# Optimization experiments

Hardware: AMD Instinct MI355X
Metric: run time of the kernel (lower is better)

The kernel has to match this reference:

```python
import jax, jax.numpy as jnp
import numpy as np

# Dims (see init_kwargs / input_specs)
B = 16            # decode batch (slots)
QH = 32           # query heads
KVH = 8           # kv heads (GQA group = QH // KVH = 4)
D = 128           # head dim
NUM_PAGES = 4096  # total pages in cache pool
TPP = 16          # tokens per page
MAX_PPS = 256     # max pages per slot -> max context 4096


def setup_inputs() -> dict:
    key = jax.random.key(0)
    k1, k2, k3, k4, k5 = jax.random.split(key, 5)
    query = jax.random.normal(k1, (B, 1, QH, D), dtype=jnp.float32)
    key_pages = jax.random.normal(k2, (KVH, NUM_PAGES, TPP, D), dtype=jnp.float32)
    value_pages = jax.random.normal(k3, (KVH, NUM_PAGES, TPP, D), dtype=jnp.float32)
    # lengths in [1, MAX_PPS*TPP) so every slot has at least one valid token
    sequence_lengths = jax.random.randint(k4, (B,), 1, MAX_PPS * TPP, dtype=jnp.int32)
    page_map = jax.random.randint(k5, (B, MAX_PPS), 0, NUM_PAGES, dtype=jnp.int32)
    return {
        "query": query,
        "key_pages": key_pages,
        "value_pages": value_pages,
        "sequence_lengths": sequence_lengths,
        "page_map": page_map,
    }


def reference(query, key_pages, value_pages, sequence_lengths, page_map):
    """Paged attention, autoregressive decode mode (q_len == 1).

    Matches pallas paged_attention semantics: gather KV pages via page_map,
    attend over the first sequence_lengths[b] tokens (no internal 1/sqrt(d)
    scaling, matching the kernel which expects a pre-scaled query).
    """
    q = jnp.squeeze(query, axis=1)
    G = QH // KVH
    q = q.reshape(B, KVH, G, D)               # GQA grouping: [B, KVH, G, D]

    # Page-table gather: [KVH, B, MAX_PPS, TPP, D] -> [B, KVH, T, D], T = MAX_PPS*TPP
    T = MAX_PPS * TPP
    k = jnp.moveaxis(key_pages[:, page_map], 1, 0).reshape(B, KVH, T, D)
    v = jnp.moveaxis(value_pages[:, page_map], 1, 0).reshape(B, KVH, T, D)

    scores = jnp.einsum("bkgd,bktd->bkgt", q, k)       # [B, KVH, G, T]
    valid = jnp.arange(T, dtype=jnp.int32)[None, :] < sequence_lengths[:, None]  # [B, T]
    neg = jnp.asarray(jnp.finfo(scores.dtype).min, scores.dtype)
    scores = jnp.where(valid[:, None, None, :], scores, neg)
    weights = jax.nn.softmax(scores, axis=-1)
    out = jnp.einsum("bkgt,bktd->bkgd", weights, v)    # [B, KVH, G, D]
    return out.reshape(B, QH, D)
```

## Files before the change

### kernel.cpp

```cpp
#include <hip/hip_runtime.h>

constexpr int B = 16;
constexpr int QH = 32;
constexpr int KVH = 8;
constexpr int G = 4;
constexpr int D = 128;
constexpr int NUM_PAGES = 4096;
constexpr int TPP = 16;
constexpr int MAX_PPS = 256;
constexpr int CHUNK = 256;
constexpr int NCHUNK = (MAX_PPS * TPP) / CHUNK;
constexpr int PPC = CHUNK / TPP;
constexpr int WSSTRIDE = D + 2;

#define NEGF (-3.0e38f)

#define RED32(p)                 \
  do {                           \
    p += __shfl_xor(p, 16);      \
    p += __shfl_xor(p, 8);       \
    p += __shfl_xor(p, 4);       \
    p += __shfl_xor(p, 2);       \
    p += __shfl_xor(p, 1);       \
  } while (0)

__global__ __launch_bounds__(256, 4)
void pa_partial(const float* __restrict__ qg, const float* __restrict__ kp,
                const float* __restrict__ vp, const int* __restrict__ lens,
                const int* __restrict__ pmap, float* __restrict__ ws) {
  const int c = blockIdx.x;
  const int kvh = blockIdx.y;
  const int b = blockIdx.z;
  const int start = c * CHUNK;
  int ntok = lens[b] - start;
  if (ntok <= 0) return;
  if (ntok > CHUNK) ntok = CHUNK;

  __shared__ int pages[PPC];
  __shared__ float sc[CHUNK * G];
  __shared__ float wred[4][4];
  __shared__ float sred[4][4];
  __shared__ float ared[4][G * D];

  const int tid = threadIdx.x;
  const int wave = tid >> 6;
  const int lane = tid & 63;
  const int half = lane >> 5;
  const int l32 = lane & 31;

  if (tid < PPC) pages[tid] = pmap[b * MAX_PPS + (start >> 4) + tid];
#pragma unroll
  for (int i = tid; i < CHUNK * G; i += 256) sc[i] = NEGF;
  __syncthreads();

  const float4 q0 = *(const float4*)(qg + (size_t)(b * QH + kvh * G + 0) * D + 4 * l32);
  const float4 q1 = *(const float4*)(qg + (size_t)(b * QH + kvh * G + 1) * D + 4 * l32);
  const float4 q2 = *(const float4*)(qg + (size_t)(b * QH + kvh * G + 2) * D + 4 * l32);
  const float4 q3 = *(const float4*)(qg + (size_t)(b * QH + kvh * G + 3) * D + 4 * l32);

  const size_t hoff = (size_t)kvh * NUM_PAGES * TPP * D;
  const float* kbase = kp + hoff;
  const float* vbase = vp + hoff;

  float m0 = NEGF, m1 = NEGF, m2 = NEGF, m3 = NEGF;

  const int iters = (ntok + 7) >> 3;
  const int tbase = wave * 2 + half;

  float4 kv = make_float4(0.f, 0.f, 0.f, 0.f);
  if (tbase < ntok) {
    const int pg = pages[tbase >> 4];
    kv = *(const float4*)(kbase + ((size_t)pg * TPP + (tbase & 15)) * D + 4 * l32);
  }
  for (int j = 0; j < iters; ++j) {
    const int t = j * 8 + tbase;
    const bool valid = (t < ntok);
    const float4 cur = kv;
    const int tn = t + 8;
    if (tn < ntok) {
      const int pg = pages[tn >> 4];
      kv = *(const float4*)(kbase + ((size_t)pg * TPP + (tn & 15)) * D + 4 * l32);
    }
    float p0 = cur.x * q0.x + cur.y * q0.y + cur.z * q0.z + cur.w * q0.w;
    float p1 = cur.x * q1.x + cur.y * q1.y + cur.z * q1.z + cur.w * q1.w;
    float p2 = cur.x * q2.x + cur.y * q2.y + cur.z * q2.z + cur.w * q2.w;
    float p3 = cur.x * q3.x + cur.y * q3.y + cur.z * q3.z + cur.w * q3.w;
    RED32(p0);
    RED32(p1);
    RED32(p2);
    RED32(p3);
    if (valid) {
      m0 = fmaxf(m0, p0);
      m1 = fmaxf(m1, p1);
      m2 = fmaxf(m2, p2);
      m3 = fmaxf(m3, p3);
      if (l32 == 0) *(float4*)(sc + t * G) = make_float4(p0, p1, p2, p3);
    }
  }
  m0 = fmaxf(m0, __shfl_xor(m0, 32));
  m1 = fmaxf(m1, __shfl_xor(m1, 32));
  m2 = fmaxf(m2, __shfl_xor(m2, 32));
  m3 = fmaxf(m3, __shfl_xor(m3, 32));
  if (lane == 0) {
    wred[wave][0] = m0;
    wred[wave][1] = m1;
    wred[wave][2] = m2;
    wred[wave][3] = m3;
  }
  __syncthreads();

  const float M0 = fmaxf(fmaxf(wred[0][0], wred[1][0]), fmaxf(wred[2][0], wred[3][0]));
  const float M1 = fmaxf(fmaxf(wred[0][1], wred[1][1]), fmaxf(wred[2][1], wred[3][1]));
  const float M2 = fmaxf(fmaxf(wred[0][2], wred[1][2]), fmaxf(wred[2][2], wred[3][2]));
  const float M3 = fmaxf(fmaxf(wred[0][3], wred[1][3]), fmaxf(wred[2][3], wred[3][3]));
  const float Ma = (tid & 1) ? M1 : M0;
  const float Mb = (tid & 1) ? M3 : M2;
  const float Mg = (tid & 2) ? Mb : Ma;

  float lsum = 0.f;
#pragma unroll
  for (int i = tid; i < CHUNK * G; i += 256) {
    const float e = __expf(sc[i] - Mg);
    sc[i] = e;
    lsum += e;
  }
  lsum += __shfl_xor(lsum, 4);
  lsum += __shfl_xor(lsum, 8);
  lsum += __shfl_xor(lsum, 16);
  lsum += __shfl_xor(lsum, 32);
  if (lane < 4) sred[wave][lane] = lsum;
  __syncthreads();

  float4 a0 = make_float4(0.f, 0.f, 0.f, 0.f);
  float4 a1 = a0, a2 = a0, a3 = a0;
  float4 vv = make_float4(0.f, 0.f, 0.f, 0.f);
  if (tbase < ntok) {
    const int pg = pages[tbase >> 4];
    vv = *(const float4*)(vbase + ((size_t)pg * TPP + (tbase & 15)) * D + 4 * l32);
  }
  for (int j = 0; j < iters; ++j) {
    const int t = j * 8 + tbase;
    const bool valid = (t < ntok);
    const float4 cur = vv;
    const int tn = t + 8;
    if (tn < ntok) {
      const int pg = pages[tn >> 4];
      vv = *(const float4*)(vbase + ((size_t)pg * TPP + (tn & 15)) * D + 4 * l32);
    }
    if (valid) {
      const float4 wv = *(const float4*)(sc + t * G);
      a0.x += wv.x * cur.x; a0.y += wv.x * cur.y; a0.z += wv.x * cur.z; a0.w += wv.x * cur.w;
      a1.x += wv.y * cur.x; a1.y += wv.y * cur.y; a1.z += wv.y * cur.z; a1.w += wv.y * cur.w;
      a2.x += wv.z * cur.x; a2.y += wv.z * cur.y; a2.z += wv.z * cur.z; a2.w += wv.z * cur.w;
      a3.x += wv.w * cur.x; a3.y += wv.w * cur.y; a3.z += wv.w * cur.z; a3.w += wv.w * cur.w;
    }
  }
  a0.x += __shfl_xor(a0.x, 32); a0.y += __shfl_xor(a0.y, 32);
  a0.z += __shfl_xor(a0.z, 32); a0.w += __shfl_xor(a0.w, 32);
  a1.x += __shfl_xor(a1.x, 32); a1.y += __shfl_xor(a1.y, 32);
  a1.z += __shfl_xor(a1.z, 32); a1.w += __shfl_xor(a1.w, 32);
  a2.x += __shfl_xor(a2.x, 32); a2.y += __shfl_xor(a2.y, 32);
  a2.z += __shfl_xor(a2.z, 32); a2.w += __shfl_xor(a2.w, 32);
  a3.x += __shfl_xor(a3.x, 32); a3.y += __shfl_xor(a3.y, 32);
  a3.z += __shfl_xor(a3.z, 32); a3.w += __shfl_xor(a3.w, 32);
  if (half == 0) {
    *(float4*)(ared[wave] + 0 * D + 4 * l32) = a0;
    *(float4*)(ared[wave] + 1 * D + 4 * l32) = a1;
    *(float4*)(ared[wave] + 2 * D + 4 * l32) = a2;
    *(float4*)(ared[wave] + 3 * D + 4 * l32) = a3;
  }
  __syncthreads();

  const size_t wsbase = ((size_t)((b * KVH + kvh) * NCHUNK + c) * G) * WSSTRIDE;
#pragma unroll
  for (int r = 0; r < 2; ++r) {
    const int idx = tid + r * 256;
    const int g = idx >> 7;
    const int d = idx & 127;
    const float v =
        ared[0][g * D + d] + ared[1][g * D + d] + ared[2][g * D + d] + ared[3][g * D + d];
    ws[wsbase + (size_t)g * WSSTRIDE + 2 + d] = v;
  }
  if (tid < 4) {
    ws[wsbase + (size_t)tid * WSSTRIDE + 0] = Mg;
    ws[wsbase + (size_t)tid * WSSTRIDE + 1] =
        sred[0][tid] + sred[1][tid] + sred[2][tid] + sred[3][tid];
  }
}

__global__ __launch_bounds__(128)
void pa_reduce(const float* __restrict__ ws, const int* __restrict__ lens,
               float* __restrict__ out) {
  const int g = blockIdx.x;
  const int kvh = blockIdx.y;
  const int b = blockIdx.z;
  const int d = threadIdx.x;
  const int nc = (lens[b] + CHUNK - 1) / CHUNK;
  float M = NEGF, L = 0.f, acc = 0.f;
  for (int c = 0; c < nc; ++c) {
    const float* p =
        ws + ((size_t)((b * KVH + kvh) * NCHUNK + c) * G + g) * WSSTRIDE;
    const float mc = p[0];
    const float lc = p[1];
    const float ac = p[2 + d];
    const float Mn = fmaxf(M, mc);
    const float so = __expf(M - Mn);
    const float se = __expf(mc - Mn);
    L = L * so + lc * se;
    acc = acc * so + ac * se;
    M = Mn;
  }
  out[(size_t)(b * QH + kvh * G + g) * D + d] = acc / L;
}

extern "C" void kernel_launch(void* const* d_in, const int* in_sizes, int n_in,
                              void* d_out, int out_size, void* d_ws, size_t ws_size,
                              hipStream_t stream) {
  (void)in_sizes; (void)n_in; (void)out_size; (void)ws_size;
  const float* q = (const float*)d_in[0];
  const float* kp = (const float*)d_in[1];
  const float* vp = (const float*)d_in[2];
  const int* lens = (const int*)d_in[3];
  const int* pmap = (const int*)d_in[4];
  float* out = (float*)d_out;
  float* ws = (float*)d_ws;

  dim3 g1(NCHUNK, KVH, B);
  pa_partial<<<g1, 256, 0, stream>>>(q, kp, vp, lens, pmap, ws);
  dim3 g2(G, KVH, B);
  pa_reduce<<<g2, 128, 0, stream>>>(ws, lens, out);
}
```

Before: 475.1 us.

## Fuse K and V passes into single-pass online softmax with lazy rescale and grid swizzle

Replaces the two-pass scheme (score all keys into shared memory, then exponentiate and accumulate V) with a single pass that loads K and V together and keeps per-wave online-softmax state. The running max is rescaled only when a new score exceeds it by more than a threshold, which avoids most rescale exponentials. Prefetch now runs two tokens ahead for both K and V. The grid is flattened and swizzled so that batch slots rotate across chunks, spreading work from unequal sequence lengths more evenly over the machine. The cost is higher register pressure and clamped page reads past the valid range, since loads are now unconditional.

```diff
diff --git a/kernel.cpp b/kernel.cpp
--- a/kernel.cpp
+++ b/kernel.cpp
@@ -14,6 +14,7 @@
 constexpr int WSSTRIDE = D + 2;
 
 #define NEGF (-3.0e38f)
+#define DEFER_T 8.0f
 
 #define RED32(p)                 \
   do {                           \
@@ -28,16 +29,19 @@
 void pa_partial(const float* __restrict__ qg, const float* __restrict__ kp,
                 const float* __restrict__ vp, const int* __restrict__ lens,
                 const int* __restrict__ pmap, float* __restrict__ ws) {
-  const int c = blockIdx.x;
-  const int kvh = blockIdx.y;
-  const int b = blockIdx.z;
+  const int f = blockIdx.x;
+  const int hi = f >> 7;
+  const int lo = f & 127;
+  const int b = ((lo & 15) + hi) & 15;
+  const int kvh = lo >> 4;
+  const int c = hi;
+
   const int start = c * CHUNK;
   int ntok = lens[b] - start;
   if (ntok <= 0) return;
   if (ntok > CHUNK) ntok = CHUNK;
 
   __shared__ int pages[PPC];
-  __shared__ float sc[CHUNK * G];
   __shared__ float wred[4][4];
   __shared__ float sred[4][4];
   __shared__ float ared[4][G * D];
@@ -49,8 +53,6 @@
   const int l32 = lane & 31;
 
   if (tid < PPC) pages[tid] = pmap[b * MAX_PPS + (start >> 4) + tid];
-#pragma unroll
-  for (int i = tid; i < CHUNK * G; i += 256) sc[i] = NEGF;
   __syncthreads();
 
   const float4 q0 = *(const float4*)(qg + (size_t)(b * QH + kvh * G + 0) * D + 4 * l32);
@@ -62,112 +64,112 @@
   const float* kbase = kp + hoff;
   const float* vbase = vp + hoff;
 
-  float m0 = NEGF, m1 = NEGF, m2 = NEGF, m3 = NEGF;
-
   const int iters = (ntok + 7) >> 3;
   const int tbase = wave * 2 + half;
 
-  float4 kv = make_float4(0.f, 0.f, 0.f, 0.f);
-  if (tbase < ntok) {
-    const int pg = pages[tbase >> 4];
-    kv = *(const float4*)(kbase + ((size_t)pg * TPP + (tbase & 15)) * D + 4 * l32);
-  }
+  auto kvoff = [&](int t) -> size_t {
+    const int pi = min(t >> 4, PPC - 1);
+    return ((size_t)pages[pi] * TPP + (t & 15)) * D + 4 * l32;
+  };
+
+  float m0 = NEGF, m1 = NEGF, m2 = NEGF, m3 = NEGF;
+  float l0 = 0.f, l1 = 0.f, l2 = 0.f, l3 = 0.f;
+  float4 a0 = make_float4(0.f, 0.f, 0.f, 0.f);
+  float4 a1 = a0, a2 = a0, a3 = a0;
+
+  size_t o = kvoff(tbase);
+  float4 kA = *(const float4*)(kbase + o);
+  float4 vA = *(const float4*)(vbase + o);
+  o = kvoff(tbase + 8);
+  float4 kB = *(const float4*)(kbase + o);
+  float4 vB = *(const float4*)(vbase + o);
+
   for (int j = 0; j < iters; ++j) {
-    const int t = j * 8 + tbase;
+    const int t = tbase + 8 * j;
     const bool valid = (t < ntok);
-    const float4 cur = kv;
-    const int tn = t + 8;
-    if (tn < ntok) {
-      const int pg = pages[tn >> 4];
-      kv = *(const float4*)(kbase + ((size_t)pg * TPP + (tn & 15)) * D + 4 * l32);
-    }
-    float p0 = cur.x * q0.x + cur.y * q0.y + cur.z * q0.z + cur.w * q0.w;
-    float p1 = cur.x * q1.x + cur.y * q1.y + cur.z * q1.z + cur.w * q1.w;
-    float p2 = cur.x * q2.x + cur.y * q2.y + cur.z * q2.z + cur.w * q2.w;
-    float p3 = cur.x * q3.x + cur.y * q3.y + cur.z * q3.z + cur.w * q3.w;
+    const float4 ck = kA, cv = vA;
+    kA = kB; vA = vB;
+    o = kvoff(tbase + 8 * (j + 2));
+    kB = *(const float4*)(kbase + o);
+    vB = *(const float4*)(vbase + o);
+
+    float p0 = ck.x * q0.x + ck.y * q0.y + ck.z * q0.z + ck.w * q0.w;
+    float p1 = ck.x * q1.x + ck.y * q1.y + ck.z * q1.z + ck.w * q1.w;
+    float p2 = ck.x * q2.x + ck.y * q2.y + ck.z * q2.z + ck.w * q2.w;
+    float p3 = ck.x * q3.x + ck.y * q3.y + ck.z * q3.z + ck.w * q3.w;
     RED32(p0);
     RED32(p1);
     RED32(p2);
     RED32(p3);
+
     if (valid) {
-      m0 = fmaxf(m0, p0);
-      m1 = fmaxf(m1, p1);
-      m2 = fmaxf(m2, p2);
-      m3 = fmaxf(m3, p3);
-      if (l32 == 0) *(float4*)(sc + t * G) = make_float4(p0, p1, p2, p3);
+      const float dmax = fmaxf(fmaxf(p0 - m0, p1 - m1), fmaxf(p2 - m2, p3 - m3));
+      if (dmax > DEFER_T) {
+        const float n0 = fmaxf(m0, p0), n1 = fmaxf(m1, p1);
+        const float n2 = fmaxf(m2, p2), n3 = fmaxf(m3, p3);
+        const float s0 = __expf(m0 - n0), s1 = __expf(m1 - n1);
+        const float s2 = __expf(m2 - n2), s3 = __expf(m3 - n3);
+        l0 *= s0; l1 *= s1; l2 *= s2; l3 *= s3;
+        a0.x *= s0; a0.y *= s0; a0.z *= s0; a0.w *= s0;
+        a1.x *= s1; a1.y *= s1; a1.z *= s1; a1.w *= s1;
+        a2.x *= s2; a2.y *= s2; a2.z *= s2; a2.w *= s2;
+        a3.x *= s3; a3.y *= s3; a3.z *= s3; a3.w *= s3;
+        m0 = n0; m1 = n1; m2 = n2; m3 = n3;
+      }
+      const float e0 = __expf(p0 - m0);
+      const float e1 = __expf(p1 - m1);
+      const float e2 = __expf(p2 - m2);
+      const float e3 = __expf(p3 - m3);
+      l0 += e0; l1 += e1; l2 += e2; l3 += e3;
+      a0.x += e0 * cv.x; a0.y += e0 * cv.y; a0.z += e0 * cv.z; a0.w += e0 * cv.w;
+      a1.x += e1 * cv.x; a1.y += e1 * cv.y; a1.z += e1 * cv.z; a1.w += e1 * cv.w;
+      a2.x += e2 * cv.x; a2.y += e2 * cv.y; a2.z += e2 * cv.z; a2.w += e2 * cv.w;
+      a3.x += e3 * cv.x; a3.y += e3 * cv.y; a3.z += e3 * cv.z; a3.w += e3 * cv.w;
     }
   }
-  m0 = fmaxf(m0, __shfl_xor(m0, 32));
-  m1 = fmaxf(m1, __shfl_xor(m1, 32));
-  m2 = fmaxf(m2, __shfl_xor(m2, 32));
-  m3 = fmaxf(m3, __shfl_xor(m3, 32));
+
+#define HMERGE(m, l, a)                                                   \
+  do {                                                                    \
+    const float pm = __shfl_xor(m, 32), pl = __shfl_xor(l, 32);           \
+    float4 pa;                                                            \
+    pa.x = __shfl_xor(a.x, 32); pa.y = __shfl_xor(a.y, 32);               \
+    pa.z = __shfl_xor(a.z, 32); pa.w = __shfl_xor(a.w, 32);               \
+    const float M = fmaxf(m, pm);                                         \
+    const float sa = __expf(m - M), sb = __expf(pm - M);                  \
+    l = l * sa + pl * sb;                                                 \
+    a.x = a.x * sa + pa.x * sb; a.y = a.y * sa + pa.y * sb;               \
+    a.z = a.z * sa + pa.z * sb; a.w = a.w * sa + pa.w * sb;               \
+    m = M;                                                                \
+  } while (0)
+  HMERGE(m0, l0, a0);
+  HMERGE(m1, l1, a1);
+  HMERGE(m2, l2, a2);
+  HMERGE(m3, l3, a3);
+#undef HMERGE
+
   if (lane == 0) {
-    wred[wave][0] = m0;
-    wred[wave][1] = m1;
-    wred[wave][2] = m2;
-    wred[wave][3] = m3;
+    wred[wave][0] = m0; wred[wave][1] = m1; wred[wave][2] = m2; wred[wave][3] = m3;
   }
   __syncthreads();
-
   const float M0 = fmaxf(fmaxf(wred[0][0], wred[1][0]), fmaxf(wred[2][0], wred[3][0]));
   const float M1 = fmaxf(fmaxf(wred[0][1], wred[1][1]), fmaxf(wred[2][1], wred[3][1]));
   const float M2 = fmaxf(fmaxf(wred[0][2], wred[1][2]), fmaxf(wred[2][2], wred[3][2]));
   const float M3 = fmaxf(fmaxf(wred[0][3], wred[1][3]), fmaxf(wred[2][3], wred[3][3]));
-  const float Ma = (tid & 1) ? M1 : M0;
-  const float Mb = (tid & 1) ? M3 : M2;
-  const float Mg = (tid & 2) ? Mb : Ma;
-
-  float lsum = 0.f;
-#pragma unroll
-  for (int i = tid; i < CHUNK * G; i += 256) {
-    const float e = __expf(sc[i] - Mg);
-    sc[i] = e;
-    lsum += e;
-  }
-  lsum += __shfl_xor(lsum, 4);
-  lsum += __shfl_xor(lsum, 8);
-  lsum += __shfl_xor(lsum, 16);
-  lsum += __shfl_xor(lsum, 32);
-  if (lane < 4) sred[wave][lane] = lsum;
-  __syncthreads();
-
-  float4 a0 = make_float4(0.f, 0.f, 0.f, 0.f);
-  float4 a1 = a0, a2 = a0, a3 = a0;
-  float4 vv = make_float4(0.f, 0.f, 0.f, 0.f);
-  if (tbase < ntok) {
-    const int pg = pages[tbase >> 4];
-    vv = *(const float4*)(vbase + ((size_t)pg * TPP + (tbase & 15)) * D + 4 * l32);
-  }
-  for (int j = 0; j < iters; ++j) {
-    const int t = j * 8 + tbase;
-    const bool valid = (t < ntok);
-    const float4 cur = vv;
-    const int tn = t + 8;
-    if (tn < ntok) {
-      const int pg = pages[tn >> 4];
-      vv = *(const float4*)(vbase + ((size_t)pg * TPP + (tn & 15)) * D + 4 * l32);
-    }
-    if (valid) {
-      const float4 wv = *(const float4*)(sc + t * G);
-      a0.x += wv.x * cur.x; a0.y += wv.x * cur.y; a0.z += wv.x * cur.z; a0.w += wv.x * cur.w;
-      a1.x += wv.y * cur.x; a1.y += wv.y * cur.y; a1.z += wv.y * cur.z; a1.w += wv.y * cur.w;
-      a2.x += wv.z * cur.x; a2.y += wv.z * cur.y; a2.z += wv.z * cur.z; a2.w += wv.z * cur.w;
-      a3.x += wv.w * cur.x; a3.y += wv.w * cur.y; a3.z += wv.w * cur.z; a3.w += wv.w * cur.w;
-    }
-  }
-  a0.x += __shfl_xor(a0.x, 32); a0.y += __shfl_xor(a0.y, 32);
-  a0.z += __shfl_xor(a0.z, 32); a0.w += __shfl_xor(a0.w, 32);
-  a1.x += __shfl_xor(a1.x, 32); a1.y += __shfl_xor(a1.y, 32);
-  a1.z += __shfl_xor(a1.z, 32); a1.w += __shfl_xor(a1.w, 32);
-  a2.x += __shfl_xor(a2.x, 32); a2.y += __shfl_xor(a2.y, 32);
-  a2.z += __shfl_xor(a2.z, 32); a2.w += __shfl_xor(a2.w, 32);
-  a3.x += __shfl_xor(a3.x, 32); a3.y += __shfl_xor(a3.y, 32);
-  a3.z += __shfl_xor(a3.z, 32); a3.w += __shfl_xor(a3.w, 32);
+  const float s0 = __expf(m0 - M0), s1 = __expf(m1 - M1);
+  const float s2 = __expf(m2 - M2), s3 = __expf(m3 - M3);
   if (half == 0) {
-    *(float4*)(ared[wave] + 0 * D + 4 * l32) = a0;
-    *(float4*)(ared[wave] + 1 * D + 4 * l32) = a1;
-    *(float4*)(ared[wave] + 2 * D + 4 * l32) = a2;
-    *(float4*)(ared[wave] + 3 * D + 4 * l32) = a3;
+    *(float4*)(ared[wave] + 0 * D + 4 * l32) =
+        make_float4(a0.x * s0, a0.y * s0, a0.z * s0, a0.w * s0);
+    *(float4*)(ared[wave] + 1 * D + 4 * l32) =
+        make_float4(a1.x * s1, a1.y * s1, a1.z * s1, a1.w * s1);
+    *(float4*)(ared[wave] + 2 * D + 4 * l32) =
+        make_float4(a2.x * s2, a2.y * s2, a2.z * s2, a2.w * s2);
+    *(float4*)(ared[wave] + 3 * D + 4 * l32) =
+        make_float4(a3.x * s3, a3.y * s3, a3.z * s3, a3.w * s3);
+  }
+  if (lane == 0) {
+    sred[wave][0] = l0 * s0; sred[wave][1] = l1 * s1;
+    sred[wave][2] = l2 * s2; sred[wave][3] = l3 * s3;
   }
   __syncthreads();
 
@@ -182,6 +184,9 @@
     ws[wsbase + (size_t)g * WSSTRIDE + 2 + d] = v;
   }
   if (tid < 4) {
+    const float Ma = (tid & 1) ? M1 : M0;
+    const float Mb = (tid & 1) ? M3 : M2;
+    const float Mg = (tid & 2) ? Mb : Ma;
     ws[wsbase + (size_t)tid * WSSTRIDE + 0] = Mg;
     ws[wsbase + (size_t)tid * WSSTRIDE + 1] =
         sred[0][tid] + sred[1][tid] + sred[2][tid] + sred[3][tid];
@@ -225,8 +230,7 @@
   float* out = (float*)d_out;
   float* ws = (float*)d_ws;
 
-  dim3 g1(NCHUNK, KVH, B);
-  pa_partial<<<g1, 256, 0, stream>>>(q, kp, vp, lens, pmap, ws);
+  pa_partial<<<NCHUNK * KVH * B, 256, 0, stream>>>(q, kp, vp, lens, pmap, ws);
   dim3 g2(G, KVH, B);
   pa_reduce<<<g2, 128, 0, stream>>>(ws, lens, out);
 }
```

After: 471.8 us. No clear change (-0.7%).
